# Performance work log

Hardware: AMD Instinct MI355X
Metric: run time of the kernel (lower is better)

The kernel has to match this reference:

```python
import jax, jax.numpy as jnp
import numpy as np

B, N, D, H, QV = 8, 1024, 64, 4, 32
C = 2 * D + 1          # combined_dim = 129
K = C // 8             # per-head qk dim = 16
M_PER = 512
M = B * M_PER
NEG = -9e15


def setup_inputs() -> dict:
    key = jax.random.key(0)
    ks = jax.random.split(key, 24)
    s = 0.05
    x = jax.random.normal(ks[0], (B, N, D + 1), jnp.float32)
    h = jax.random.normal(ks[1], (B, N, D), jnp.float32)
    query_vectors = jax.random.normal(ks[2], (M, QV), jnp.float32)
    adj = jax.random.randint(ks[3], (N, N), 0, 2, jnp.int32)
    # unique observed nodes per graph (mimics torch.where on an obs mask)
    perm = jax.vmap(lambda k: jax.random.permutation(k, N))(jax.random.split(ks[4], B))
    nodes_n = perm[:, :M_PER].reshape(-1).astype(jnp.int32)
    nodes_b = jnp.repeat(jnp.arange(B, dtype=jnp.int32), M_PER)
    # per-head attention projections, stacked over heads
    Wq = jax.random.normal(ks[5], (H, C, K), jnp.float32) * s
    bq = jax.random.normal(ks[6], (H, K), jnp.float32) * s
    Wk = jax.random.normal(ks[7], (H, C, K), jnp.float32) * s
    bk = jax.random.normal(ks[8], (H, K), jnp.float32) * s
    Wv = jax.random.normal(ks[9], (H, C, C), jnp.float32) * s
    bv = jax.random.normal(ks[10], (H, C), jnp.float32) * s
    # attentionMLP: Linear(H*C, C) -> ReLU -> Linear(C, C)
    W1 = jax.random.normal(ks[11], (H * C, C), jnp.float32) * s
    b1 = jax.random.normal(ks[12], (C,), jnp.float32) * s
    W2 = jax.random.normal(ks[13], (C, C), jnp.float32) * s
    b2 = jax.random.normal(ks[14], (C,), jnp.float32) * s
    # MLP_Param hypernetwork tensors: W[qvd, in=C, out=D], b[qvd, D]
    Wr = jax.random.normal(ks[15], (QV, C, D), jnp.float32) * s
    br = jax.random.normal(ks[16], (QV, D), jnp.float32) * s
    Wu = jax.random.normal(ks[17], (QV, C, D), jnp.float32) * s
    bu = jax.random.normal(ks[18], (QV, D), jnp.float32) * s
    Wc = jax.random.normal(ks[19], (QV, C, D), jnp.float32) * s
    bc = jax.random.normal(ks[20], (QV, D), jnp.float32) * s
    return dict(x=x, h=h, query_vectors=query_vectors, adj=adj,
                nodes_b=nodes_b, nodes_n=nodes_n,
                Wq=Wq, bq=bq, Wk=Wk, bk=bk, Wv=Wv, bv=bv,
                W1=W1, b1=b1, W2=W2, b2=b2,
                Wr=Wr, br=br, Wu=Wu, bu=bu, Wc=Wc, bc=bc)


def _mlp_param(sel, qv, W, b):
    # hypernetwork: per-node generated linear layer
    Wn = jnp.einsum('md,dio->mio', qv, W)   # [M, C, D]
    bn = qv @ b                              # [M, D]
    return jnp.einsum('mi,mio->mo', sel, Wn) + bn


def reference(x, h, query_vectors, adj, nodes_b, nodes_n,
              Wq, bq, Wk, bk, Wv, bv, W1, b1, W2, b2,
              Wr, br, Wu, bu, Wc, bc):
    combined = jnp.concatenate([x, h], axis=-1)                      # [B,N,C]
    q = jnp.einsum('bnc,hck->hbnk', combined, Wq) + bq[:, None, None, :]
    k = jnp.einsum('bnc,hck->hbnk', combined, Wk) + bk[:, None, None, :]
    v = jnp.einsum('bnc,hcd->hbnd', combined, Wv) + bv[:, None, None, :]
    scores = jnp.einsum('hbnk,hbmk->hbnm', q, k) / jnp.sqrt(jnp.float32(K))
    scores = jax.nn.leaky_relu(scores, 0.2)
    scores = jnp.where(adj == 0, NEG, scores)                        # [N,N] broadcast
    attn = jax.nn.softmax(scores, axis=-1)                           # [H,B,N,N]
    hp = jnp.einsum('hbnm,hbmd->hbnd', attn, v)                      # [H,B,N,C]
    # permute(1,2,0,3).reshape -> concat heads per node
    attn_cat = jnp.transpose(hp, (1, 2, 0, 3)).reshape(B, N, H * C)
    mlp_out = jax.nn.relu(attn_cat @ W1 + b1) @ W2 + b2              # [B,N,C]
    combined = mlp_out + combined                                    # skip connection
    sel = combined[nodes_b, nodes_n]                                 # [M,C]
    r = jax.nn.sigmoid(_mlp_param(sel, query_vectors, Wr, br))       # [M,D]
    u = jax.nn.sigmoid(_mlp_param(sel, query_vectors, Wu, bu))       # [M,D]
    h = h.at[nodes_b, nodes_n].set(r * h[nodes_b, nodes_n])
    combined_new = jnp.concatenate([x, h], axis=-1)
    cand = jnp.tanh(_mlp_param(combined_new[nodes_b, nodes_n], query_vectors, Wc, bc))
    new_h = (1.0 - u) * h[nodes_b, nodes_n] + u * cand               # [M,D]
    return new_h
```

## Files before the change

kernel.cpp:

```cpp
#include <hip/hip_runtime.h>

#define DEVINL __device__ __forceinline__

typedef unsigned short ushort_t;
typedef __attribute__((ext_vector_type(8))) short short8;
typedef __attribute__((ext_vector_type(8))) unsigned short ushort8;
typedef __attribute__((ext_vector_type(4))) float f32x4;

constexpr int B_ = 8, N_ = 1024, D_ = 64, H_ = 4, QV_ = 32;
constexpr int C_ = 129, K_ = 16, M_ = 4096;
constexpr int CP = 132;
constexpr int NG = B_ * N_;
constexpr int CBS = 160;
constexpr int VTN = 144;
constexpr int KT = 4256;
constexpr int NKT = 133;
constexpr int HPS = 544;

constexpr size_t o_cb    = 0;
constexpr size_t o_q     = o_cb  + (size_t)NG * CBS / 2;
constexpr size_t o_k     = o_q   + (size_t)H_ * NG * K_;
constexpr size_t o_wqk   = o_k   + (size_t)H_ * NG * K_;
constexpr size_t o_wvt   = o_wqk + (size_t)H_ * 32 * CBS / 2;
constexpr size_t o_vT    = o_wvt + (size_t)H_ * VTN * CBS / 2;
constexpr size_t o_hpb   = o_vT  + (size_t)H_ * VTN * NG / 2;
constexpr size_t o_cpost = o_hpb + (size_t)M_ * HPS / 2;
constexpr size_t o_W1T   = o_cpost + (size_t)M_ * CP;
constexpr size_t o_W2T   = o_W1T + (size_t)144 * HPS / 2;
constexpr size_t o_wtru  = o_W2T + (size_t)144 * 160 / 2;
constexpr size_t o_wtc   = o_wtru + (size_t)128 * KT / 2;
constexpr size_t o_A     = o_wtc + (size_t)64 * KT / 2;
constexpr size_t o_pru   = o_A + (size_t)M_ * KT / 2;
constexpr size_t o_pc2   = o_pru + (size_t)4 * M_ * 128;
constexpr size_t o_cin = o_q;

DEVINL float4 ld4(const float* p) { return *reinterpret_cast<const float4*>(p); }
DEVINL void st4(float* p, float4 v) { *reinterpret_cast<float4*>(p) = v; }
DEVINL ushort_t f2bf(float f) {
    unsigned int u = __float_as_uint(f);
    u += 0x7FFFu + ((u >> 16) & 1u);
    return (ushort_t)(u >> 16);
}

__global__ void k_comb(const float* __restrict__ x, const float* __restrict__ h,
                       ushort_t* __restrict__ cb) {
    int idx = blockIdx.x * 256 + threadIdx.x;
    if (idx >= NG * CBS) return;
    int g = idx / CBS, kk = idx - g * CBS;
    float v;
    if (kk < 65) v = x[g * 65 + kk];
    else if (kk < 129) v = h[g * 64 + (kk - 65)];
    else if (kk == 129) v = 1.0f;
    else v = 0.f;
    cb[idx] = f2bf(v);
}

__global__ void k_wqkv(const float* __restrict__ Wq, const float* __restrict__ bq,
                       const float* __restrict__ Wk, const float* __restrict__ bk,
                       const float* __restrict__ Wv, const float* __restrict__ bv,
                       ushort_t* __restrict__ wqk, ushort_t* __restrict__ wvt) {
    int idx = blockIdx.x * 256 + threadIdx.x;
    const int tot1 = H_ * 32 * CBS;
    const int tot2 = H_ * VTN * CBS;
    if (idx < tot1) {
        int hh = idx / (32 * CBS); int rem = idx - hh * 32 * CBS;
        int o = rem / CBS, kk = rem - o * CBS;
        float v = 0.f;
        if (o < 16) {
            if (kk < 129) v = Wq[(size_t)(hh * C_ + kk) * K_ + o];
            else if (kk == 129) v = bq[hh * K_ + o];
        } else {
            int o2 = o - 16;
            if (kk < 129) v = Wk[(size_t)(hh * C_ + kk) * K_ + o2];
            else if (kk == 129) v = bk[hh * K_ + o2];
        }
        wqk[idx] = f2bf(v);
    } else if (idx < tot1 + tot2) {
        int j = idx - tot1;
        int hh = j / (VTN * CBS); int rem = j - hh * VTN * CBS;
        int n = rem / CBS, kk = rem - n * CBS;
        float v = 0.f;
        if (n < C_) {
            if (kk < 129) v = Wv[(size_t)(hh * C_ + kk) * C_ + n];
            else if (kk == 129) v = bv[hh * C_ + n];
        }
        wvt[j] = f2bf(v);
    }
}

__global__ void k_wmlp(const float* __restrict__ W1, const float* __restrict__ W2,
                       ushort_t* __restrict__ W1T, ushort_t* __restrict__ W2T) {
    int idx = blockIdx.x * 256 + threadIdx.x;
    const int tot1 = 144 * HPS;
    const int tot2 = 144 * 160;
    if (idx < tot1) {
        int o = idx / HPS, k = idx - o * HPS;
        float v = (o < C_ && k < 516) ? W1[(size_t)k * C_ + o] : 0.f;
        W1T[idx] = f2bf(v);
    } else if (idx < tot1 + tot2) {
        int j = idx - tot1;
        int o = j / 160, k = j - o * 160;
        float v = (o < C_ && k < C_) ? W2[(size_t)k * C_ + o] : 0.f;
        W2T[j] = f2bf(v);
    }
}

__global__ void k_wt(const float* __restrict__ Wr, const float* __restrict__ br,
                     const float* __restrict__ Wu, const float* __restrict__ bu,
                     const float* __restrict__ Wc, const float* __restrict__ bc,
                     ushort_t* __restrict__ wtru, ushort_t* __restrict__ wtc) {
    int idx = blockIdx.x * 256 + threadIdx.x;
    const int tot = 192 * KT;
    if (idx >= tot) return;
    int row = idx / KT, k = idx - row * KT;
    float v;
    if (k >= 4224) {
        int d = k - 4224;
        if (row < 64) v = br[d * 64 + row];
        else if (row < 128) v = bu[d * 64 + row - 64];
        else v = bc[d * 64 + row - 128];
    } else {
        int d = k / 132, i = k - d * 132;
        if (i >= 129) v = 0.f;
        else if (row < 64) v = Wr[(size_t)(d * 129 + i) * 64 + row];
        else if (row < 128) v = Wu[(size_t)(d * 129 + i) * 64 + row - 64];
        else v = Wc[(size_t)(d * 129 + i) * 64 + row - 128];
    }
    if (row < 128) wtru[(size_t)row * KT + k] = f2bf(v);
    else wtc[(size_t)(row - 128) * KT + k] = f2bf(v);
}

__global__ __launch_bounds__(256) void k_qkv(
    const ushort_t* __restrict__ cb, const ushort_t* __restrict__ wqk,
    const ushort_t* __restrict__ wvt,
    float* __restrict__ qo, float* __restrict__ ko, ushort_t* __restrict__ vTg) {
    const int t = threadIdx.x;
    const int g0 = blockIdx.x * 16;
    const int hh = blockIdx.y;
    const int lane = t & 63, w = t >> 6;
    const int am = lane & 15, aq = lane >> 4;
    short8 cbf[5];
    const ushort_t* Cr = cb + (size_t)(g0 + am) * CBS + aq * 8;
#pragma unroll
    for (int kt = 0; kt < 5; ++kt)
        cbf[kt] = *reinterpret_cast<const short8*>(Cr + kt * 32);
#pragma unroll
    for (int s = 0; s < 3; ++s) {
        int u = w + 4 * s;
        if (u >= 11) break;
        f32x4 acc = f32x4{0.f, 0.f, 0.f, 0.f};
        if (u < 2) {
            const ushort_t* Bp = wqk + ((size_t)(hh * 32 + u * 16 + am)) * CBS + aq * 8;
#pragma unroll
            for (int kt = 0; kt < 5; ++kt)
                acc = __builtin_amdgcn_mfma_f32_16x16x32_bf16(
                    cbf[kt], *reinterpret_cast<const short8*>(Bp + kt * 32), acc, 0, 0, 0);
            float* dst = u ? ko : qo;
#pragma unroll
            for (int i = 0; i < 4; ++i)
                dst[(size_t)(hh * NG + g0 + aq * 4 + i) * K_ + am] = acc[i];
        } else {
            int vt = u - 2;
            const ushort_t* Ap = wvt + ((size_t)(hh * VTN + vt * 16 + am)) * CBS + aq * 8;
#pragma unroll
            for (int kt = 0; kt < 5; ++kt)
                acc = __builtin_amdgcn_mfma_f32_16x16x32_bf16(
                    *reinterpret_cast<const short8*>(Ap + kt * 32), cbf[kt], acc, 0, 0, 0);
#pragma unroll
            for (int i = 0; i < 4; ++i)
                vTg[(size_t)(hh * VTN + vt * 16 + aq * 4 + i) * NG + g0 + am] = f2bf(acc[i]);
        }
    }
}

__global__ __launch_bounds__(256) void k_attn(
    const float* __restrict__ qg, const float* __restrict__ kg,
    const ushort_t* __restrict__ vTg,
    const int* __restrict__ adj, const int* __restrict__ nodes_b, const int* __restrict__ nodes_n,
    ushort_t* __restrict__ hpb) {
    __shared__ alignas(16) float Ks[64 * 20];
    __shared__ alignas(16) ushort_t Vt[VTN * 72];
    __shared__ alignas(16) ushort_t Pb[16 * 72];
    __shared__ float Lrow[16];
    __shared__ int Nrow[16];
    const int t = threadIdx.x;
    const int m0 = blockIdx.x * 16;
    const int hh = blockIdx.y;
    const int b = nodes_b[m0];
    if (t < 16) Nrow[t] = nodes_n[m0 + t];
    __syncthreads();
    const int r = t >> 4, cl = t & 15;
    float qreg[16];
    {
        const float* qp = &qg[(size_t)(hh * NG + b * N_ + Nrow[r]) * K_];
#pragma unroll
        for (int w4 = 0; w4 < 16; w4 += 4) {
            float4 qq = ld4(qp + w4);
            qreg[w4] = qq.x; qreg[w4 + 1] = qq.y; qreg[w4 + 2] = qq.z; qreg[w4 + 3] = qq.w;
        }
    }
    const int* adjrow = &adj[(size_t)Nrow[r] * N_];
    const int lane = t & 63, w = t >> 6;
    const int am = lane & 15, aq = lane >> 4;
    f32x4 accv[5];
#pragma unroll
    for (int s = 0; s < 5; ++s) accv[s] = f32x4{0.f, 0.f, 0.f, 0.f};
    float lsum = 0.f;

    for (int ct = 0; ct < 16; ++ct) {
        const int c0 = ct * 64;
        __syncthreads();
        {
            int row = t >> 2, k4 = (t & 3) * 4;
            st4(&Ks[row * 20 + k4], ld4(&kg[(size_t)(hh * NG + b * N_ + c0 + row) * K_ + k4]));
        }
        for (int idx = t; idx < VTN * 8; idx += 256) {
            int n = idx >> 3, l8 = idx & 7;
            *reinterpret_cast<ushort8*>(&Vt[n * 72 + l8 * 8]) =
                *reinterpret_cast<const ushort8*>(&vTg[(size_t)(hh * VTN + n) * NG + b * N_ + c0 + l8 * 8]);
        }
        __syncthreads();
#pragma unroll
        for (int j = 0; j < 4; ++j) {
            int c = cl + 16 * j;
            const float* kc = &Ks[c * 20];
            float4 k0 = ld4(kc), k1 = ld4(kc + 4), k2 = ld4(kc + 8), k3 = ld4(kc + 12);
            float dot = qreg[0]*k0.x + qreg[1]*k0.y + qreg[2]*k0.z + qreg[3]*k0.w
                      + qreg[4]*k1.x + qreg[5]*k1.y + qreg[6]*k1.z + qreg[7]*k1.w
                      + qreg[8]*k2.x + qreg[9]*k2.y + qreg[10]*k2.z + qreg[11]*k2.w
                      + qreg[12]*k3.x + qreg[13]*k3.y + qreg[14]*k3.z + qreg[15]*k3.w;
            float s = dot * 0.25f;
            s = (s >= 0.f) ? s : 0.2f * s;
            float p = adjrow[c0 + c] ? __expf(s) : 0.f;
            lsum += p;
            Pb[r * 72 + c] = f2bf(p);
        }
        __syncthreads();
#pragma unroll
        for (int s = 0; s < 5; ++s) {
            int u = 4 * s + w;
            if (u < 18) {
                int nt = u >> 1, kh = u & 1;
                short8 af = *reinterpret_cast<const short8*>(&Pb[am * 72 + kh * 32 + aq * 8]);
                short8 bfr = *reinterpret_cast<const short8*>(&Vt[(nt * 16 + am) * 72 + kh * 32 + aq * 8]);
                accv[s] = __builtin_amdgcn_mfma_f32_16x16x32_bf16(af, bfr, accv[s], 0, 0, 0);
            }
        }
    }
    lsum += __shfl_xor(lsum, 1);
    lsum += __shfl_xor(lsum, 2);
    lsum += __shfl_xor(lsum, 4);
    lsum += __shfl_xor(lsum, 8);
    if (cl == 0) Lrow[r] = lsum;
    __syncthreads();
    float* Ored = reinterpret_cast<float*>(Vt);
    if (w & 1) {
#pragma unroll
        for (int s = 0; s < 5; ++s) {
            int u = 4 * s + w;
            if (u < 18) {
                int nt = u >> 1;
#pragma unroll
                for (int i = 0; i < 4; ++i)
                    Ored[(aq * 4 + i) * 160 + nt * 16 + am] = accv[s][i];
            }
        }
    }
    if (t < 16) Lrow[t] = (Lrow[t] > 0.f) ? 1.f / Lrow[t] : 0.f;
    __syncthreads();
    if (!(w & 1)) {
#pragma unroll
        for (int s = 0; s < 5; ++s) {
            int u = 4 * s + w;
            if (u < 18) {
                int nt = u >> 1;
                int col = nt * 16 + am;
                if (col < C_) {
#pragma unroll
                    for (int i = 0; i < 4; ++i) {
                        int row = aq * 4 + i;
                        float val = (accv[s][i] + Ored[row * 160 + col]) * Lrow[row];
                        hpb[(size_t)(m0 + row) * HPS + hh * C_ + col] = f2bf(val);
                    }
                }
            }
        }
    }
    if (hh == 3) {
        for (int idx = t; idx < 16 * 28; idx += 256) {
            int rr = idx / 28, cc = 516 + (idx - rr * 28);
            hpb[(size_t)(m0 + rr) * HPS + cc] = 0;
        }
    }
}

__global__ __launch_bounds__(256) void k_mlp(
    const ushort_t* __restrict__ hpb,
    const ushort_t* __restrict__ W1T, const float* __restrict__ b1,
    const ushort_t* __restrict__ W2T, const float* __restrict__ b2,
    const float* __restrict__ x, const float* __restrict__ h,
    const int* __restrict__ nb, const int* __restrict__ nn,
    float* __restrict__ cpost) {
    __shared__ alignas(16) ushort_t Hs[16 * 168];
    const int t = threadIdx.x;
    const int m0 = blockIdx.x * 16;
    const int lane = t & 63, w = t >> 6;
    const int am = lane & 15, aq = lane >> 4;
    f32x4 acc[3];
#pragma unroll
    for (int j = 0; j < 3; ++j) acc[j] = f32x4{0.f, 0.f, 0.f, 0.f};
    const ushort_t* Ar = hpb + (size_t)(m0 + am) * HPS;
    for (int kt = 0; kt < 17; ++kt) {
        short8 af = *reinterpret_cast<const short8*>(Ar + kt * 32 + aq * 8);
#pragma unroll
        for (int j = 0; j < 3; ++j) {
            int nt = w + 4 * j;
            if (nt < 9) {
                short8 bf = *reinterpret_cast<const short8*>(W1T + (size_t)(nt * 16 + am) * HPS + kt * 32 + aq * 8);
                acc[j] = __builtin_amdgcn_mfma_f32_16x16x32_bf16(af, bf, acc[j], 0, 0, 0);
            }
        }
    }
#pragma unroll
    for (int j = 0; j < 3; ++j) {
        int nt = w + 4 * j;
        if (nt < 9) {
            int col = nt * 16 + am;
            float bb = (col < C_) ? b1[col] : 0.f;
#pragma unroll
            for (int i = 0; i < 4; ++i) {
                int row = aq * 4 + i;
                float v = (col < C_) ? fmaxf(acc[j][i] + bb, 0.f) : 0.f;
                Hs[row * 168 + col] = f2bf(v);
            }
        }
    }
    { int row = t >> 4, cc = 144 + (t & 15); Hs[row * 168 + cc] = 0; }
    __syncthreads();
    f32x4 acc2[3];
#pragma unroll
    for (int j = 0; j < 3; ++j) acc2[j] = f32x4{0.f, 0.f, 0.f, 0.f};
    for (int kt = 0; kt < 5; ++kt) {
        short8 af = *reinterpret_cast<const short8*>(&Hs[am * 168 + kt * 32 + aq * 8]);
#pragma unroll
        for (int j = 0; j < 3; ++j) {
            int nt = w + 4 * j;
            if (nt < 9) {
                short8 bf = *reinterpret_cast<const short8*>(W2T + (size_t)(nt * 16 + am) * 160 + kt * 32 + aq * 8);
                acc2[j] = __builtin_amdgcn_mfma_f32_16x16x32_bf16(af, bf, acc2[j], 0, 0, 0);
            }
        }
    }
#pragma unroll
    for (int j = 0; j < 3; ++j) {
        int nt = w + 4 * j;
        if (nt < 9) {
            int col = nt * 16 + am;
            if (col < C_) {
                float bb = b2[col];
#pragma unroll
                for (int i = 0; i < 4; ++i) {
                    int m = m0 + aq * 4 + i;
                    int b = nb[m], n = nn[m];
                    float sk = (col < 65) ? x[(b * N_ + n) * 65 + col]
                                          : h[(b * N_ + n) * D_ + (col - 65)];
                    cpost[(size_t)m * CP + col] = acc2[j][i] + bb + sk;
                }
            }
        }
    }
    if (t < 48) {
        int rr = t / 3, cc = 129 + (t - (t / 3) * 3);
        cpost[(size_t)(m0 + rr) * CP + cc] = 0.f;
    }
}

__global__ __launch_bounds__(256) void k_arow(const float* __restrict__ src,
                                              const float* __restrict__ qv,
                                              ushort_t* __restrict__ A) {
    __shared__ float sq[CP];
    __shared__ float qs[QV_];
    const int t = threadIdx.x;
    const int m = blockIdx.x;
    if (t < CP) sq[t] = src[(size_t)m * CP + t];
    if (t >= 224) qs[t - 224] = qv[m * QV_ + (t - 224)];
    __syncthreads();
    ushort_t* Ar = A + (size_t)m * KT;
    for (int k = t; k < 4224; k += 256) {
        int d = k / 132, i = k - d * 132;
        Ar[k] = f2bf(qs[d] * sq[i]);
    }
    if (t < QV_) Ar[4224 + t] = f2bf(qs[t]);
}

template<int NN>
__global__ __launch_bounds__(256) void k_gemm(const ushort_t* __restrict__ A,
                                              const ushort_t* __restrict__ WT,
                                              float* __restrict__ part) {
    const int t = threadIdx.x;
    const int m0 = blockIdx.x * 16;
    const int z = blockIdx.y;
    const int lane = t & 63, w = t >> 6;
    const int am = lane & 15, aq = lane >> 4;
    constexpr int NTpW = NN / 64;
    const int ktb = z * 34;
    const int kte = (ktb + 34 < NKT) ? ktb + 34 : NKT;
    f32x4 acc[NTpW];
#pragma unroll
    for (int j = 0; j < NTpW; ++j) acc[j] = f32x4{0.f, 0.f, 0.f, 0.f};
    const ushort_t* Ar = A + (size_t)(m0 + am) * KT;
    for (int kt = ktb; kt < kte; ++kt) {
        const int ko = kt * 32 + aq * 8;
        short8 af = *reinterpret_cast<const short8*>(Ar + ko);
#pragma unroll
        for (int j = 0; j < NTpW; ++j) {
            int nt = w + 4 * j;
            short8 bf = *reinterpret_cast<const short8*>(WT + (size_t)(nt * 16 + am) * KT + ko);
            acc[j] = __builtin_amdgcn_mfma_f32_16x16x32_bf16(af, bf, acc[j], 0, 0, 0);
        }
    }
#pragma unroll
    for (int j = 0; j < NTpW; ++j) {
        int n = (w + 4 * j) * 16 + am;
#pragma unroll
        for (int i = 0; i < 4; ++i) {
            int m = m0 + aq * 4 + i;
            part[((size_t)z * M_ + m) * NN + n] = acc[j][i];
        }
    }
}

__global__ void k_build_cin(const float* __restrict__ x, const float* __restrict__ h,
                            const int* __restrict__ nb, const int* __restrict__ nn,
                            const float* __restrict__ pru, float* __restrict__ cin) {
    int idx = blockIdx.x * 256 + threadIdx.x;
    if (idx >= M_ * CP) return;
    int m = idx / CP, i = idx - m * CP;
    int b = nb[m], n = nn[m];
    float val;
    if (i < 65) val = x[(b * N_ + n) * 65 + i];
    else if (i < C_) {
        int o = i - 65;
        const size_t S = (size_t)M_ * 128;
        size_t base = (size_t)m * 128 + o;
        float s = pru[base] + pru[S + base] + pru[2 * S + base] + pru[3 * S + base];
        float rv = 1.f / (1.f + __expf(-s));
        val = rv * h[(b * N_ + n) * D_ + o];
    } else val = 0.f;
    cin[idx] = val;
}

__global__ void k_final(const float* __restrict__ pru, const float* __restrict__ pc,
                        const float* __restrict__ cin, float* __restrict__ out) {
    int idx = blockIdx.x * 256 + threadIdx.x;
    if (idx >= M_ * D_) return;
    int m = idx >> 6, o = idx & 63;
    const size_t Su = (size_t)M_ * 128;
    size_t bu = (size_t)m * 128 + 64 + o;
    float su = pru[bu] + pru[Su + bu] + pru[2 * Su + bu] + pru[3 * Su + bu];
    float uv = 1.f / (1.f + __expf(-su));
    const size_t Sc = (size_t)M_ * 64;
    size_t bc = (size_t)m * 64 + o;
    float sc = pc[bc] + pc[Sc + bc] + pc[2 * Sc + bc] + pc[3 * Sc + bc];
    float cand = tanhf(sc);
    float hn = cin[(size_t)m * CP + 65 + o];
    out[idx] = (1.f - uv) * hn + uv * cand;
}

extern "C" void kernel_launch(void* const* d_in, const int* in_sizes, int n_in,
                              void* d_out, int out_size, void* d_ws, size_t ws_size,
                              hipStream_t stream) {
    const float* x   = (const float*)d_in[0];
    const float* h   = (const float*)d_in[1];
    const float* qv  = (const float*)d_in[2];
    const int*   adj = (const int*)d_in[3];
    const int*   nb  = (const int*)d_in[4];
    const int*   nn  = (const int*)d_in[5];
    const float* Wq  = (const float*)d_in[6];
    const float* bq  = (const float*)d_in[7];
    const float* Wk  = (const float*)d_in[8];
    const float* bk  = (const float*)d_in[9];
    const float* Wv  = (const float*)d_in[10];
    const float* bv  = (const float*)d_in[11];
    const float* W1  = (const float*)d_in[12];
    const float* b1  = (const float*)d_in[13];
    const float* W2  = (const float*)d_in[14];
    const float* b2  = (const float*)d_in[15];
    const float* Wr  = (const float*)d_in[16];
    const float* br  = (const float*)d_in[17];
    const float* Wu  = (const float*)d_in[18];
    const float* bu  = (const float*)d_in[19];
    const float* Wc  = (const float*)d_in[20];
    const float* bc  = (const float*)d_in[21];
    float* ws = (float*)d_ws;
    float* out = (float*)d_out;

    ushort_t* cb   = (ushort_t*)(ws + o_cb);
    float* qo    = ws + o_q;
    float* ko    = ws + o_k;
    ushort_t* wqk  = (ushort_t*)(ws + o_wqk);
    ushort_t* wvt  = (ushort_t*)(ws + o_wvt);
    ushort_t* vTg  = (ushort_t*)(ws + o_vT);
    ushort_t* hpb  = (ushort_t*)(ws + o_hpb);
    float* cpost = ws + o_cpost;
    ushort_t* W1T  = (ushort_t*)(ws + o_W1T);
    ushort_t* W2T  = (ushort_t*)(ws + o_W2T);
    ushort_t* wtru = (ushort_t*)(ws + o_wtru);
    ushort_t* wtc  = (ushort_t*)(ws + o_wtc);
    ushort_t* Abuf = (ushort_t*)(ws + o_A);
    float* pru   = ws + o_pru;
    float* pc    = ws + o_pc2;
    float* cin   = ws + o_cin;

    k_comb<<<(NG * CBS + 255) / 256, 256, 0, stream>>>(x, h, cb);
    k_wqkv<<<(H_ * 32 * CBS + H_ * VTN * CBS + 255) / 256, 256, 0, stream>>>(
        Wq, bq, Wk, bk, Wv, bv, wqk, wvt);
    k_wmlp<<<(144 * HPS + 144 * 160 + 255) / 256, 256, 0, stream>>>(W1, W2, W1T, W2T);
    k_wt<<<(192 * KT + 255) / 256, 256, 0, stream>>>(Wr, br, Wu, bu, Wc, bc, wtru, wtc);
    k_qkv<<<dim3(NG / 16, H_), 256, 0, stream>>>(cb, wqk, wvt, qo, ko, vTg);
    k_attn<<<dim3(M_ / 16, H_), 256, 0, stream>>>(qo, ko, vTg, adj, nb, nn, hpb);
    k_mlp<<<M_ / 16, 256, 0, stream>>>(hpb, W1T, b1, W2T, b2, x, h, nb, nn, cpost);
    k_arow<<<M_, 256, 0, stream>>>(cpost, qv, Abuf);
    k_gemm<128><<<dim3(M_ / 16, 4), 256, 0, stream>>>(Abuf, wtru, pru);
    k_build_cin<<<(M_ * CP) / 256, 256, 0, stream>>>(x, h, nb, nn, pru, cin);
    k_arow<<<M_, 256, 0, stream>>>(cin, qv, Abuf);
    k_gemm<64><<<dim3(M_ / 16, 4), 256, 0, stream>>>(Abuf, wtc, pc);
    k_final<<<(M_ * D_) / 256, 256, 0, stream>>>(pru, pc, cin, out);
}
```

Measured before the change: 295.9 us.

## Restructure attention with MFMA scores, bit-packed adjacency, and per-wave key splits

Measured after the change: 296.1 us. No clear change (+0.1%).

```diff
diff --git a/kernel.cpp b/kernel.cpp
--- a/kernel.cpp
+++ b/kernel.cpp
@@ -3,6 +3,7 @@
 #define DEVINL __device__ __forceinline__
 
 typedef unsigned short ushort_t;
+typedef unsigned long long u64;
 typedef __attribute__((ext_vector_type(8))) short short8;
 typedef __attribute__((ext_vector_type(8))) unsigned short ushort8;
 typedef __attribute__((ext_vector_type(4))) float f32x4;
@@ -18,9 +19,10 @@
 constexpr int HPS = 544;
 
 constexpr size_t o_cb    = 0;
-constexpr size_t o_q     = o_cb  + (size_t)NG * CBS / 2;
-constexpr size_t o_k     = o_q   + (size_t)H_ * NG * K_;
-constexpr size_t o_wqk   = o_k   + (size_t)H_ * NG * K_;
+constexpr size_t o_qb    = o_cb  + (size_t)NG * CBS / 2;
+constexpr size_t o_kb    = o_qb  + (size_t)H_ * NG * 16 / 2;
+constexpr size_t o_adjb  = o_kb  + (size_t)H_ * NG * 16 / 2;
+constexpr size_t o_wqk   = o_adjb + 32768;
 constexpr size_t o_wvt   = o_wqk + (size_t)H_ * 32 * CBS / 2;
 constexpr size_t o_vT    = o_wvt + (size_t)H_ * VTN * CBS / 2;
 constexpr size_t o_hpb   = o_vT  + (size_t)H_ * VTN * NG / 2;
@@ -32,7 +34,7 @@
 constexpr size_t o_A     = o_wtc + (size_t)64 * KT / 2;
 constexpr size_t o_pru   = o_A + (size_t)M_ * KT / 2;
 constexpr size_t o_pc2   = o_pru + (size_t)4 * M_ * 128;
-constexpr size_t o_cin = o_q;
+constexpr size_t o_cin = o_vT;
 
 DEVINL float4 ld4(const float* p) { return *reinterpret_cast<const float4*>(p); }
 DEVINL void st4(float* p, float4 v) { *reinterpret_cast<float4*>(p) = v; }
@@ -53,6 +55,14 @@
     else if (kk == 129) v = 1.0f;
     else v = 0.f;
     cb[idx] = f2bf(v);
+}
+
+__global__ void k_adjb(const int* __restrict__ adj, u64* __restrict__ ab) {
+    int word = blockIdx.x * 4 + (threadIdx.x >> 6);
+    int lane = threadIdx.x & 63;
+    int row = word >> 4, wj = word & 15;
+    u64 m = __ballot(adj[(size_t)row * N_ + wj * 64 + lane] != 0);
+    if (lane == 0) ab[word] = m;
 }
 
 __global__ void k_wqkv(const float* __restrict__ Wq, const float* __restrict__ bq,
@@ -133,7 +143,7 @@
 __global__ __launch_bounds__(256) void k_qkv(
     const ushort_t* __restrict__ cb, const ushort_t* __restrict__ wqk,
     const ushort_t* __restrict__ wvt,
-    float* __restrict__ qo, float* __restrict__ ko, ushort_t* __restrict__ vTg) {
+    ushort_t* __restrict__ qbo, ushort_t* __restrict__ kbo, ushort_t* __restrict__ vTg) {
     const int t = threadIdx.x;
     const int g0 = blockIdx.x * 16;
     const int hh = blockIdx.y;
@@ -155,10 +165,10 @@
             for (int kt = 0; kt < 5; ++kt)
                 acc = __builtin_amdgcn_mfma_f32_16x16x32_bf16(
                     cbf[kt], *reinterpret_cast<const short8*>(Bp + kt * 32), acc, 0, 0, 0);
-            float* dst = u ? ko : qo;
+            ushort_t* dst = u ? kbo : qbo;
 #pragma unroll
             for (int i = 0; i < 4; ++i)
-                dst[(size_t)(hh * NG + g0 + aq * 4 + i) * K_ + am] = acc[i];
+                dst[(size_t)(hh * NG + g0 + aq * 4 + i) * 16 + am] = f2bf(acc[i]);
         } else {
             int vt = u - 2;
             const ushort_t* Ap = wvt + ((size_t)(hh * VTN + vt * 16 + am)) * CBS + aq * 8;
@@ -174,14 +184,15 @@
 }
 
 __global__ __launch_bounds__(256) void k_attn(
-    const float* __restrict__ qg, const float* __restrict__ kg,
-    const ushort_t* __restrict__ vTg,
-    const int* __restrict__ adj, const int* __restrict__ nodes_b, const int* __restrict__ nodes_n,
+    const ushort_t* __restrict__ qb, const ushort_t* __restrict__ kb,
+    const ushort_t* __restrict__ vTg, const u64* __restrict__ adjb,
+    const int* __restrict__ nodes_b, const int* __restrict__ nodes_n,
     ushort_t* __restrict__ hpb) {
-    __shared__ alignas(16) float Ks[64 * 20];
-    __shared__ alignas(16) ushort_t Vt[VTN * 72];
-    __shared__ alignas(16) ushort_t Pb[16 * 72];
-    __shared__ float Lrow[16];
+    __shared__ u64 Msk[16][16];
+    __shared__ alignas(16) ushort_t Pb[4][16 * 72];
+    __shared__ float Ored[3][16 * 144];
+    __shared__ float Lpart[4][16];
+    __shared__ float Linv[16];
     __shared__ int Nrow[16];
     const int t = threadIdx.x;
     const int m0 = blockIdx.x * 16;
@@ -189,99 +200,82 @@
     const int b = nodes_b[m0];
     if (t < 16) Nrow[t] = nodes_n[m0 + t];
     __syncthreads();
-    const int r = t >> 4, cl = t & 15;
-    float qreg[16];
-    {
-        const float* qp = &qg[(size_t)(hh * NG + b * N_ + Nrow[r]) * K_];
-#pragma unroll
-        for (int w4 = 0; w4 < 16; w4 += 4) {
-            float4 qq = ld4(qp + w4);
-            qreg[w4] = qq.x; qreg[w4 + 1] = qq.y; qreg[w4 + 2] = qq.z; qreg[w4 + 3] = qq.w;
-        }
-    }
-    const int* adjrow = &adj[(size_t)Nrow[r] * N_];
+    { int r = t >> 4, wj = t & 15; Msk[r][wj] = adjb[Nrow[r] * 16 + wj]; }
     const int lane = t & 63, w = t >> 6;
     const int am = lane & 15, aq = lane >> 4;
-    f32x4 accv[5];
-#pragma unroll
-    for (int s = 0; s < 5; ++s) accv[s] = f32x4{0.f, 0.f, 0.f, 0.f};
-    float lsum = 0.f;
-
-    for (int ct = 0; ct < 16; ++ct) {
-        const int c0 = ct * 64;
-        __syncthreads();
-        {
-            int row = t >> 2, k4 = (t & 3) * 4;
-            st4(&Ks[row * 20 + k4], ld4(&kg[(size_t)(hh * NG + b * N_ + c0 + row) * K_ + k4]));
-        }
-        for (int idx = t; idx < VTN * 8; idx += 256) {
-            int n = idx >> 3, l8 = idx & 7;
-            *reinterpret_cast<ushort8*>(&Vt[n * 72 + l8 * 8]) =
-                *reinterpret_cast<const ushort8*>(&vTg[(size_t)(hh * VTN + n) * NG + b * N_ + c0 + l8 * 8]);
-        }
-        __syncthreads();
-#pragma unroll
-        for (int j = 0; j < 4; ++j) {
-            int c = cl + 16 * j;
-            const float* kc = &Ks[c * 20];
-            float4 k0 = ld4(kc), k1 = ld4(kc + 4), k2 = ld4(kc + 8), k3 = ld4(kc + 12);
-            float dot = qreg[0]*k0.x + qreg[1]*k0.y + qreg[2]*k0.z + qreg[3]*k0.w
-                      + qreg[4]*k1.x + qreg[5]*k1.y + qreg[6]*k1.z + qreg[7]*k1.w
-                      + qreg[8]*k2.x + qreg[9]*k2.y + qreg[10]*k2.z + qreg[11]*k2.w
-                      + qreg[12]*k3.x + qreg[13]*k3.y + qreg[14]*k3.z + qreg[15]*k3.w;
-            float s = dot * 0.25f;
-            s = (s >= 0.f) ? s : 0.2f * s;
-            float p = adjrow[c0 + c] ? __expf(s) : 0.f;
-            lsum += p;
-            Pb[r * 72 + c] = f2bf(p);
-        }
-        __syncthreads();
-#pragma unroll
-        for (int s = 0; s < 5; ++s) {
-            int u = 4 * s + w;
-            if (u < 18) {
-                int nt = u >> 1, kh = u & 1;
-                short8 af = *reinterpret_cast<const short8*>(&Pb[am * 72 + kh * 32 + aq * 8]);
-                short8 bfr = *reinterpret_cast<const short8*>(&Vt[(nt * 16 + am) * 72 + kh * 32 + aq * 8]);
-                accv[s] = __builtin_amdgcn_mfma_f32_16x16x32_bf16(af, bfr, accv[s], 0, 0, 0);
-            }
-        }
-    }
-    lsum += __shfl_xor(lsum, 1);
-    lsum += __shfl_xor(lsum, 2);
-    lsum += __shfl_xor(lsum, 4);
-    lsum += __shfl_xor(lsum, 8);
-    if (cl == 0) Lrow[r] = lsum;
+    short8 qf = short8{0, 0, 0, 0, 0, 0, 0, 0};
+    if (aq < 2)
+        qf = *reinterpret_cast<const short8*>(&qb[(size_t)(hh * NG + b * N_ + Nrow[am]) * 16 + aq * 8]);
     __syncthreads();
-    float* Ored = reinterpret_cast<float*>(Vt);
-    if (w & 1) {
-#pragma unroll
-        for (int s = 0; s < 5; ++s) {
-            int u = 4 * s + w;
-            if (u < 18) {
-                int nt = u >> 1;
-#pragma unroll
-                for (int i = 0; i < 4; ++i)
-                    Ored[(aq * 4 + i) * 160 + nt * 16 + am] = accv[s][i];
-            }
-        }
-    }
-    if (t < 16) Lrow[t] = (Lrow[t] > 0.f) ? 1.f / Lrow[t] : 0.f;
+    ushort_t* Pw = Pb[w];
+    const ushort_t* kbase = kb + ((size_t)hh * NG + b * N_) * 16;
+    f32x4 accv[9];
+#pragma unroll
+    for (int j = 0; j < 9; ++j) accv[j] = f32x4{0.f, 0.f, 0.f, 0.f};
+    float lsum[4] = {0.f, 0.f, 0.f, 0.f};
+
+    for (int ti = 0; ti < 4; ++ti) {
+        const int c0 = (w + 4 * ti) * 64;
+        u64 mrow[4];
+#pragma unroll
+        for (int i = 0; i < 4; ++i) mrow[i] = Msk[aq * 4 + i][c0 >> 6];
+#pragma unroll
+        for (int nt = 0; nt < 4; ++nt) {
+            int col = c0 + nt * 16 + am;
+            short8 bf = short8{0, 0, 0, 0, 0, 0, 0, 0};
+            if (aq < 2)
+                bf = *reinterpret_cast<const short8*>(&kbase[(size_t)col * 16 + aq * 8]);
+            f32x4 sv = __builtin_amdgcn_mfma_f32_16x16x32_bf16(qf, bf, f32x4{0.f, 0.f, 0.f, 0.f}, 0, 0, 0);
+#pragma unroll
+            for (int i = 0; i < 4; ++i) {
+                float s = sv[i] * 0.25f;
+                s = (s >= 0.f) ? s : 0.2f * s;
+                float p = ((mrow[i] >> (nt * 16 + am)) & 1ull) ? __expf(s) : 0.f;
+                lsum[i] += p;
+                Pw[(aq * 4 + i) * 72 + nt * 16 + am] = f2bf(p);
+            }
+        }
+#pragma unroll
+        for (int kh = 0; kh < 2; ++kh) {
+            short8 af = *reinterpret_cast<const short8*>(&Pw[am * 72 + kh * 32 + aq * 8]);
+#pragma unroll
+            for (int nt = 0; nt < 9; ++nt) {
+                short8 bfr = *reinterpret_cast<const short8*>(
+                    &vTg[(size_t)(hh * VTN + nt * 16 + am) * NG + b * N_ + c0 + kh * 32 + aq * 8]);
+                accv[nt] = __builtin_amdgcn_mfma_f32_16x16x32_bf16(af, bfr, accv[nt], 0, 0, 0);
+            }
+        }
+    }
+#pragma unroll
+    for (int i = 0; i < 4; ++i) {
+        float v = lsum[i];
+        v += __shfl_xor(v, 1); v += __shfl_xor(v, 2);
+        v += __shfl_xor(v, 4); v += __shfl_xor(v, 8);
+        if (am == 0) Lpart[w][aq * 4 + i] = v;
+    }
+    if (w > 0) {
+#pragma unroll
+        for (int nt = 0; nt < 9; ++nt)
+#pragma unroll
+            for (int i = 0; i < 4; ++i)
+                Ored[w - 1][(aq * 4 + i) * 144 + nt * 16 + am] = accv[nt][i];
+    }
     __syncthreads();
-    if (!(w & 1)) {
-#pragma unroll
-        for (int s = 0; s < 5; ++s) {
-            int u = 4 * s + w;
-            if (u < 18) {
-                int nt = u >> 1;
-                int col = nt * 16 + am;
-                if (col < C_) {
-#pragma unroll
-                    for (int i = 0; i < 4; ++i) {
-                        int row = aq * 4 + i;
-                        float val = (accv[s][i] + Ored[row * 160 + col]) * Lrow[row];
-                        hpb[(size_t)(m0 + row) * HPS + hh * C_ + col] = f2bf(val);
-                    }
+    if (w == 0) {
+        if (t < 16) {
+            float s = Lpart[0][t] + Lpart[1][t] + Lpart[2][t] + Lpart[3][t];
+            Linv[t] = (s > 0.f) ? 1.f / s : 0.f;
+        }
+#pragma unroll
+        for (int nt = 0; nt < 9; ++nt) {
+            int col = nt * 16 + am;
+            if (col < C_) {
+#pragma unroll
+                for (int i = 0; i < 4; ++i) {
+                    int row = aq * 4 + i;
+                    float val = accv[nt][i] + Ored[0][row * 144 + col]
+                              + Ored[1][row * 144 + col] + Ored[2][row * 144 + col];
+                    hpb[(size_t)(m0 + row) * HPS + hh * C_ + col] = f2bf(val * Linv[row]);
                 }
             }
         }
@@ -496,8 +490,9 @@
     float* out = (float*)d_out;
 
     ushort_t* cb   = (ushort_t*)(ws + o_cb);
-    float* qo    = ws + o_q;
-    float* ko    = ws + o_k;
+    ushort_t* qb   = (ushort_t*)(ws + o_qb);
+    ushort_t* kb   = (ushort_t*)(ws + o_kb);
+    u64*      ab   = (u64*)(ws + o_adjb);
     ushort_t* wqk  = (ushort_t*)(ws + o_wqk);
     ushort_t* wvt  = (ushort_t*)(ws + o_wvt);
     ushort_t* vTg  = (ushort_t*)(ws + o_vT);
@@ -513,12 +508,13 @@
     float* cin   = ws + o_cin;
 
     k_comb<<<(NG * CBS + 255) / 256, 256, 0, stream>>>(x, h, cb);
+    k_adjb<<<(N_ * 16) / 4, 256, 0, stream>>>(adj, ab);
     k_wqkv<<<(H_ * 32 * CBS + H_ * VTN * CBS + 255) / 256, 256, 0, stream>>>(
         Wq, bq, Wk, bk, Wv, bv, wqk, wvt);
     k_wmlp<<<(144 * HPS + 144 * 160 + 255) / 256, 256, 0, stream>>>(W1, W2, W1T, W2T);
     k_wt<<<(192 * KT + 255) / 256, 256, 0, stream>>>(Wr, br, Wu, bu, Wc, bc, wtru, wtc);
-    k_qkv<<<dim3(NG / 16, H_), 256, 0, stream>>>(cb, wqk, wvt, qo, ko, vTg);
-    k_attn<<<dim3(M_ / 16, H_), 256, 0, stream>>>(qo, ko, vTg, adj, nb, nn, hpb);
+    k_qkv<<<dim3(NG / 16, H_), 256, 0, stream>>>(cb, wqk, wvt, qb, kb, vTg);
+    k_attn<<<dim3(M_ / 16, H_), 256, 0, stream>>>(qb, kb, vTg, ab, nb, nn, hpb);
     k_mlp<<<M_ / 16, 256, 0, stream>>>(hpb, W1T, b1, W2T, b2, x, h, nb, nn, cpost);
     k_arow<<<M_, 256, 0, stream>>>(cpost, qv, Abuf);
     k_gemm<128><<<dim3(M_ / 16, 4), 256, 0, stream>>>(Abuf, wtru, pru);
```
